# Kernel optimization log

Measured on AMD Instinct MI355X. Metric: run time of the kernel, lower is better.

## Reference

```python
import jax, jax.numpy as jnp
import numpy as np

D = 128      # state_dim
ED = 20      # edge_dim (RBF basis size)
R = 3        # num message/update rounds
G = 3        # gated equivariant blocks
CUT = 5.0    # cutoff
N = 10000    # nodes
E = 160000   # edges
B = 500      # molecules
HRO = 64     # readout hidden


def setup_inputs() -> dict:
    key = jax.random.key(0)
    ks = jax.random.split(key, 40)
    sc = 0.05

    def nrm(k, shape):
        return jax.random.normal(k, shape, dtype=jnp.float32) * sc

    inp = {
        "h": jax.random.normal(ks[0], (N, 5), dtype=jnp.float32),
        "pos": jax.random.normal(ks[1], (N, 3), dtype=jnp.float32),
        "edge_index": jax.random.randint(ks[2], (2, E), 0, N),
        "batch": jnp.sort(jax.random.randint(ks[3], (N,), 0, B)),
        # node embedding Linear(5, D)
        "emb_w": nrm(ks[4], (5, D)), "emb_b": nrm(ks[5], (D,)),
        # per-round message params (stacked over rounds)
        "msg_phi_w1": nrm(ks[6], (R, D, D)), "msg_phi_b1": nrm(ks[7], (R, D)),
        "msg_phi_w2": nrm(ks[8], (R, D, 3 * D)), "msg_phi_b2": nrm(ks[9], (R, 3 * D)),
        "msg_filt_w": nrm(ks[10], (R, ED, 3 * D)), "msg_filt_b": nrm(ks[11], (R, 3 * D)),
        # per-round update params
        "upd_U": nrm(ks[12], (R, D, D)), "upd_V": nrm(ks[13], (R, D, D)),
        "upd_w1": nrm(ks[14], (R, 2 * D, D)), "upd_b1": nrm(ks[15], (R, D)),
        "upd_w2": nrm(ks[16], (R, D, 3 * D)), "upd_b2": nrm(ks[17], (R, 3 * D)),
        # gated equivariant blocks
        "geb_wv1": nrm(ks[18], (G, D, D)), "geb_wv2": nrm(ks[19], (G, D, D)),
        "geb_w1": nrm(ks[20], (G, 2 * D, D)), "geb_b1": nrm(ks[21], (G, D)),
        "geb_w2": nrm(ks[22], (G, D, 2 * D)), "geb_b2": nrm(ks[23], (G, 2 * D)),
        # invariant readout MLP
        "ro_w1": nrm(ks[24], (D, HRO)), "ro_b1": nrm(ks[25], (HRO,)),
        "ro_w2": nrm(ks[26], (HRO, 1)), "ro_b2": nrm(ks[27], (1,)),
    }
    return inp


def _safe_norm(x, axis):
    return jnp.sqrt(jnp.sum(x * x, axis=axis) + 1e-8)


def reference(h, pos, edge_index, batch,
              emb_w, emb_b,
              msg_phi_w1, msg_phi_b1, msg_phi_w2, msg_phi_b2,
              msg_filt_w, msg_filt_b,
              upd_U, upd_V, upd_w1, upd_b1, upd_w2, upd_b2,
              geb_wv1, geb_wv2, geb_w1, geb_b1, geb_w2, geb_b2,
              ro_w1, ro_b1, ro_w2, ro_b2):
    n_nodes = h.shape[0]
    row, col = edge_index[0], edge_index[1]
    # edge vectors: r_ij = pos[col] - pos[row]
    r_ij = pos[col] - pos[row]                                   # [E,3]
    d = jnp.clip(jnp.linalg.norm(r_ij, axis=1, keepdims=True), 1e-6, None)  # [E,1]
    unit = r_ij / d                                              # [E,3]
    # sinc radial basis + cosine cutoff
    freqs = jnp.arange(1, ED + 1, dtype=h.dtype)
    rbf = jnp.sin(freqs * jnp.pi * d / CUT) / d                  # [E,ED]
    fcut = 0.5 * (jnp.cos(jnp.pi * d / CUT) + 1.0) * (d < CUT)   # [E,1]

    s = h @ emb_w + emb_b                                        # [N,D]
    v = jnp.zeros((n_nodes, D, 3), dtype=h.dtype)                # [N,D,3]

    for r in range(R):
        # --- PaiNNMessage ---
        phi = jax.nn.silu(s @ msg_phi_w1[r] + msg_phi_b1[r]) @ msg_phi_w2[r] + msg_phi_b2[r]  # [N,3D]
        filt = (rbf @ msg_filt_w[r] + msg_filt_b[r]) * fcut      # [E,3D]
        x = phi[col] * filt                                      # gather + modulate  [E,3D]
        xs, xvv, xvw = jnp.split(x, 3, axis=-1)                  # each [E,D]
        ds = jax.ops.segment_sum(xs, row, num_segments=n_nodes)  # [N,D]
        dv_e = xvv[:, :, None] * v[col] + xvw[:, :, None] * unit[:, None, :]  # [E,D,3]
        dv = jax.ops.segment_sum(dv_e, row, num_segments=n_nodes)             # [N,D,3]
        s = s + ds
        v = v + dv
        # --- PaiNNUpdate ---
        Uv = jnp.einsum('ndc,de->nec', v, upd_U[r])              # [N,D,3]
        Vv = jnp.einsum('ndc,de->nec', v, upd_V[r])              # [N,D,3]
        Vn = _safe_norm(Vv, axis=-1)                             # [N,D]
        a = jax.nn.silu(jnp.concatenate([s, Vn], axis=-1) @ upd_w1[r] + upd_b1[r]) @ upd_w2[r] + upd_b2[r]
        a_ss, a_sv, a_vv = jnp.split(a, 3, axis=-1)
        s = s + a_ss + a_sv * jnp.sum(Uv * Vv, axis=-1)
        v = v + a_vv[:, :, None] * Uv

    # --- GatedEquivariantBlocks ---
    for g in range(G):
        v1 = jnp.einsum('ndc,de->nec', v, geb_wv1[g])
        v2 = jnp.einsum('ndc,de->nec', v, geb_wv2[g])
        n2 = _safe_norm(v2, axis=-1)                             # [N,D]
        a = jax.nn.silu(jnp.concatenate([s, n2], axis=-1) @ geb_w1[g] + geb_b1[g]) @ geb_w2[g] + geb_b2[g]
        s_new, gate = jnp.split(a, 2, axis=-1)
        s = s_new
        v = gate[:, :, None] * v1

    # --- InvariantReadout + molwise scatter ---
    out = jax.nn.silu(s @ ro_w1 + ro_b1) @ ro_w2 + ro_b2         # [N,1]
    molwise = jax.ops.segment_sum(out, batch, num_segments=B)    # [B,1]
    return molwise.squeeze(-1)
```

## Files before the change

### kernel.cpp

```cpp
#include <hip/hip_runtime.h>

typedef __attribute__((ext_vector_type(4))) float f32x4;
typedef __attribute__((ext_vector_type(8))) short short8;

#define D 128
#define D3 384
#define SLD 256
#define EDIM 20
#define KPAD 32
#define NR 3
#define NG 3
#define CUTOFF 5.0f
#define NNODES 10000
#define NEDGES 160000
#define NMOL 500
#define HROH 64
#define PI_F 3.14159265358979323846f

#define FBIAS 1
#define FSILU 2
#define FBF16O 4

static __device__ __forceinline__ float silu_f(float x) {
    return x / (1.0f + expf(-x));
}

static __device__ __forceinline__ ushort f2bf(float x) {
    uint u = __float_as_uint(x);
    uint r = (u + 0x7fffu + ((u >> 16) & 1u)) >> 16;
    return (ushort)r;
}
static __device__ __forceinline__ float bf2f(ushort h) {
    return __uint_as_float((uint)h << 16);
}
static __device__ __forceinline__ uint pack2(float a, float b) {
    return (uint)f2bf(a) | ((uint)f2bf(b) << 16);
}

#define TLR 64
#define TLC 64
#define KC 32
#define APAD 40
#define BPAD 36
#define CPAD 68

struct WSrc { const float* p[12]; };
#define WTOT 880640

__global__ __launch_bounds__(256) void wprep_k(WSrc ws, ushort* __restrict__ dh,
                                               ushort* __restrict__ dl)
{
    const int srcK[12] = {128,128, 20,128,128,256,128,128,128,256,128,128};
    const int dstK[12] = {128,128, 32,128,128,256,128,128,128,256,128,128};
    const int Mm[12]   = {128,384,384,128,128,128,384,128,128,128,256, 64};
    const int nm[12]   = {  3,  3,  3,  3,  3,  3,  3,  3,  3,  3,  3,  1};
    int i = blockIdx.x * 256 + threadIdx.x;
    if (i >= WTOT) return;
    int off = 0, seg = -1, loc = 0;
    #pragma unroll
    for (int s = 0; s < 12; ++s) {
        int sz = nm[s] * Mm[s] * dstK[s];
        if (seg < 0 && i < off + sz) { seg = s; loc = i - off; }
        off += sz;
    }
    int K = dstK[seg], M = Mm[seg], sK = srcK[seg];
    int mat = loc / (M * K);
    int rem = loc - mat * M * K;
    int m = rem / K, k = rem - m * K;
    float v = (k < sK) ? ws.p[seg][(size_t)(mat * sK + k) * M + m] : 0.f;
    ushort h = f2bf(v);
    dh[i] = h;
    dl[i] = f2bf(v - bf2f(h));
}

#define SEG_PHI_W1  0
#define SEG_PHI_W2  49152
#define SEG_FILT_W  196608
#define SEG_UPD_U   233472
#define SEG_UPD_V   282624
#define SEG_UPD_W1  331776
#define SEG_UPD_W2  430080
#define SEG_GEB_WV1 577536
#define SEG_GEB_WV2 626688
#define SEG_GEB_W1  675840
#define SEG_GEB_W2  774144
#define SEG_RO_W1   872448

template <int K1, int M2, bool OUTBF>
__global__ __launch_bounds__(256) void mlp_k(
    const float* __restrict__ A, int lda,
    const ushort* __restrict__ W1h, const ushort* __restrict__ W1l,
    const float* __restrict__ b1,
    const ushort* __restrict__ W2h, const ushort* __restrict__ W2l,
    const float* __restrict__ b2,
    float* __restrict__ C, ushort* __restrict__ Cbf, int N)
{
    __shared__ char SMB[27648 + 17408];
    ushort* Ah  = (ushort*)SMB;
    ushort* Al  = Ah + 1280;
    ushort* B1h = Ah + 2560;
    ushort* B1l = B1h + 4608;
    ushort* Hh  = (ushort*)(SMB + 27648);
    ushort* Hl  = Hh + 4352;

    const int tid = threadIdx.x;
    const int n0 = blockIdx.x * 32;
    const int w = tid >> 6;
    const int rt = w & 1;
    const int ch = w >> 1;
    const int lane = tid & 63;
    const int fr = lane & 15;
    const int kg = lane >> 4;
    const int arow = tid & 31;
    const int akq = (tid >> 5) * 4;
    const bool aok = (n0 + arow) < N;
    const float* Ar = A + (size_t)(n0 + arow) * lda;
    const int bcol = tid & 127;
    const int bhalf = tid >> 7;

    f32x4 acc1[4];
    #pragma unroll
    for (int t = 0; t < 4; ++t) acc1[t] = (f32x4){0.f, 0.f, 0.f, 0.f};

    for (int k0 = 0; k0 < K1; k0 += KC) {
        {
            float4 v = aok ? *(const float4*)(Ar + k0 + akq)
                           : make_float4(0.f, 0.f, 0.f, 0.f);
            ushort h0 = f2bf(v.x), h1 = f2bf(v.y), h2 = f2bf(v.z), h3 = f2bf(v.w);
            ushort l0 = f2bf(v.x - bf2f(h0)), l1 = f2bf(v.y - bf2f(h1));
            ushort l2 = f2bf(v.z - bf2f(h2)), l3 = f2bf(v.w - bf2f(h3));
            uint2 ph, pl;
            ph.x = (uint)h0 | ((uint)h1 << 16); ph.y = (uint)h2 | ((uint)h3 << 16);
            pl.x = (uint)l0 | ((uint)l1 << 16); pl.y = (uint)l2 | ((uint)l3 << 16);
            *(uint2*)(Ah + arow * APAD + akq) = ph;
            *(uint2*)(Al + arow * APAD + akq) = pl;
        }
        {
            const ushort* sh = W1h + (size_t)bcol * K1 + k0 + bhalf * 16;
            const ushort* sl = W1l + (size_t)bcol * K1 + k0 + bhalf * 16;
            ushort* dh = B1h + bcol * BPAD + bhalf * 16;
            ushort* dl = B1l + bcol * BPAD + bhalf * 16;
            uint4 v0 = *(const uint4*)sh;
            uint4 v1 = *(const uint4*)(sh + 8);
            *(uint2*)dh       = make_uint2(v0.x, v0.y);
            *(uint2*)(dh + 4) = make_uint2(v0.z, v0.w);
            *(uint2*)(dh + 8) = make_uint2(v1.x, v1.y);
            *(uint2*)(dh + 12)= make_uint2(v1.z, v1.w);
            uint4 u0 = *(const uint4*)sl;
            uint4 u1 = *(const uint4*)(sl + 8);
            *(uint2*)dl       = make_uint2(u0.x, u0.y);
            *(uint2*)(dl + 4) = make_uint2(u0.z, u0.w);
            *(uint2*)(dl + 8) = make_uint2(u1.x, u1.y);
            *(uint2*)(dl + 12)= make_uint2(u1.z, u1.w);
        }
        __syncthreads();
        short8 ah = *(const short8*)(Ah + (rt * 16 + fr) * APAD + kg * 8);
        short8 al = *(const short8*)(Al + (rt * 16 + fr) * APAD + kg * 8);
        #pragma unroll
        for (int t = 0; t < 4; ++t) {
            const ushort* bp = B1h + (ch * 64 + t * 16 + fr) * BPAD + kg * 8;
            const ushort* bq = B1l + (ch * 64 + t * 16 + fr) * BPAD + kg * 8;
            short8 bh, bl;
            ((uint2*)&bh)[0] = *(const uint2*)bp;
            ((uint2*)&bh)[1] = *(const uint2*)(bp + 4);
            ((uint2*)&bl)[0] = *(const uint2*)bq;
            ((uint2*)&bl)[1] = *(const uint2*)(bq + 4);
            acc1[t] = __builtin_amdgcn_mfma_f32_16x16x32_bf16(ah, bh, acc1[t], 0, 0, 0);
            acc1[t] = __builtin_amdgcn_mfma_f32_16x16x32_bf16(al, bh, acc1[t], 0, 0, 0);
            acc1[t] = __builtin_amdgcn_mfma_f32_16x16x32_bf16(ah, bl, acc1[t], 0, 0, 0);
        }
        __syncthreads();
    }
    #pragma unroll
    for (int t = 0; t < 4; ++t) {
        int colm = ch * 64 + t * 16 + fr;
        float b = b1[colm];
        #pragma unroll
        for (int r = 0; r < 4; ++r) {
            int row = rt * 16 + kg * 4 + r;
            float hv = silu_f(acc1[t][r] + b);
            ushort hh = f2bf(hv);
            Hh[row * 136 + colm] = hh;
            Hl[row * 136 + colm] = f2bf(hv - bf2f(hh));
        }
    }
    __syncthreads();

    ushort* B2h = (ushort*)SMB;
    ushort* B2l = B2h + 4608;
    const int NG2 = M2 / 128;
    for (int g = 0; g < NG2; ++g) {
        f32x4 acc2[4];
        #pragma unroll
        for (int t = 0; t < 4; ++t) acc2[t] = (f32x4){0.f, 0.f, 0.f, 0.f};
        for (int k0 = 0; k0 < D; k0 += KC) {
            {
                const ushort* sh = W2h + (size_t)(g * 128 + bcol) * D + k0 + bhalf * 16;
                const ushort* sl = W2l + (size_t)(g * 128 + bcol) * D + k0 + bhalf * 16;
                ushort* dh = B2h + bcol * BPAD + bhalf * 16;
                ushort* dl = B2l + bcol * BPAD + bhalf * 16;
                uint4 v0 = *(const uint4*)sh;
                uint4 v1 = *(const uint4*)(sh + 8);
                *(uint2*)dh       = make_uint2(v0.x, v0.y);
                *(uint2*)(dh + 4) = make_uint2(v0.z, v0.w);
                *(uint2*)(dh + 8) = make_uint2(v1.x, v1.y);
                *(uint2*)(dh + 12)= make_uint2(v1.z, v1.w);
                uint4 u0 = *(const uint4*)sl;
                uint4 u1 = *(const uint4*)(sl + 8);
                *(uint2*)dl       = make_uint2(u0.x, u0.y);
                *(uint2*)(dl + 4) = make_uint2(u0.z, u0.w);
                *(uint2*)(dl + 8) = make_uint2(u1.x, u1.y);
                *(uint2*)(dl + 12)= make_uint2(u1.z, u1.w);
            }
            __syncthreads();
            short8 ah, al;
            {
                const ushort* hp = Hh + (rt * 16 + fr) * 136 + k0 + kg * 8;
                const ushort* hq = Hl + (rt * 16 + fr) * 136 + k0 + kg * 8;
                ((uint2*)&ah)[0] = *(const uint2*)hp;
                ((uint2*)&ah)[1] = *(const uint2*)(hp + 4);
                ((uint2*)&al)[0] = *(const uint2*)hq;
                ((uint2*)&al)[1] = *(const uint2*)(hq + 4);
            }
            #pragma unroll
            for (int t = 0; t < 4; ++t) {
                const ushort* bp = B2h + (ch * 64 + t * 16 + fr) * BPAD + kg * 8;
                const ushort* bq = B2l + (ch * 64 + t * 16 + fr) * BPAD + kg * 8;
                short8 bh, bl;
                ((uint2*)&bh)[0] = *(const uint2*)bp;
                ((uint2*)&bh)[1] = *(const uint2*)(bp + 4);
                ((uint2*)&bl)[0] = *(const uint2*)bq;
                ((uint2*)&bl)[1] = *(const uint2*)(bq + 4);
                acc2[t] = __builtin_amdgcn_mfma_f32_16x16x32_bf16(ah, bh, acc2[t], 0, 0, 0);
                acc2[t] = __builtin_amdgcn_mfma_f32_16x16x32_bf16(al, bh, acc2[t], 0, 0, 0);
                acc2[t] = __builtin_amdgcn_mfma_f32_16x16x32_bf16(ah, bl, acc2[t], 0, 0, 0);
            }
            __syncthreads();
        }
        if (OUTBF) {
            float* Cs = (float*)SMB;
            #pragma unroll
            for (int t = 0; t < 4; ++t) {
                int colm = ch * 64 + t * 16 + fr;
                float b = b2[g * 128 + colm];
                #pragma unroll
                for (int r = 0; r < 4; ++r) {
                    int row = rt * 16 + kg * 4 + r;
                    Cs[row * CPAD + colm] = acc2[t][r] + b;
                }
            }
            __syncthreads();
            #pragma unroll
            for (int it = 0; it < 2; ++it) {
                int chunk = it * 256 + tid;
                int row = chunk >> 4;
                int c8 = (chunk & 15) * 8;
                int n = n0 + row;
                if (n < N) {
                    const float* src = Cs + row * CPAD + c8;
                    uint4 pk;
                    pk.x = pack2(src[0], src[1]);
                    pk.y = pack2(src[2], src[3]);
                    pk.z = pack2(src[4], src[5]);
                    pk.w = pack2(src[6], src[7]);
                    *(uint4*)(Cbf + (size_t)n * M2 + g * 128 + c8) = pk;
                }
            }
            __syncthreads();
        } else {
            #pragma unroll
            for (int t = 0; t < 4; ++t) {
                int colm = ch * 64 + t * 16 + fr;
                float b = b2[g * 128 + colm];
                #pragma unroll
                for (int r = 0; r < 4; ++r) {
                    int n = n0 + rt * 16 + kg * 4 + r;
                    if (n < N)
                        C[(size_t)n * M2 + g * 128 + colm] = acc2[t][r] + b;
                }
            }
        }
    }
}

__global__ __launch_bounds__(256) void gemm_k(
    const float* __restrict__ A, int lda,
    const ushort* __restrict__ Wh, const ushort* __restrict__ Wl, int ldk,
    const float* __restrict__ bias,
    float* __restrict__ C, ushort* __restrict__ Cbf, int ldc,
    int N, int K, int flags)
{
    const int n0 = blockIdx.x * TLR;
    const int m0 = blockIdx.y * TLC;
    __shared__ ushort SM[9728];
    ushort* Ah = SM;
    ushort* Al = SM + 2560;
    ushort* Bh = SM + 5120;
    ushort* Bl = SM + 7424;
    const int tid = threadIdx.x;
    const int arow = tid & 63;
    const int akq = (tid >> 6) * 4;
    const bool aok = (n0 + arow) < N;
    const float* Ar = A + (size_t)(n0 + arow) * lda;
    const int sm = tid & 63;
    const int sq = tid >> 6;
    const ushort* Wph = Wh + (size_t)(m0 + sm) * ldk + sq * 8;
    const ushort* Wpl = Wl + (size_t)(m0 + sm) * ldk + sq * 8;
    const int lane = tid & 63;
    const int wrow = (tid >> 6) * 16;
    const int fr = lane & 15;
    const int kg = lane >> 4;

    f32x4 acc[4];
    #pragma unroll
    for (int t = 0; t < 4; ++t) acc[t] = (f32x4){0.f, 0.f, 0.f, 0.f};

    for (int k0 = 0; k0 < K; k0 += KC) {
        #pragma unroll
        for (int half = 0; half < 2; ++half) {
            int kk = akq + half * 16;
            float4 v = aok ? *(const float4*)(Ar + k0 + kk)
                           : make_float4(0.f, 0.f, 0.f, 0.f);
            ushort h0 = f2bf(v.x), h1 = f2bf(v.y), h2 = f2bf(v.z), h3 = f2bf(v.w);
            ushort l0 = f2bf(v.x - bf2f(h0)), l1 = f2bf(v.y - bf2f(h1));
            ushort l2 = f2bf(v.z - bf2f(h2)), l3 = f2bf(v.w - bf2f(h3));
            uint2 ph, pl;
            ph.x = (uint)h0 | ((uint)h1 << 16); ph.y = (uint)h2 | ((uint)h3 << 16);
            pl.x = (uint)l0 | ((uint)l1 << 16); pl.y = (uint)l2 | ((uint)l3 << 16);
            *(uint2*)(Ah + arow * APAD + kk) = ph;
            *(uint2*)(Al + arow * APAD + kk) = pl;
        }
        {
            uint4 vh = *(const uint4*)(Wph + k0);
            uint4 vl = *(const uint4*)(Wpl + k0);
            ushort* dh = Bh + sm * BPAD + sq * 8;
            ushort* dl = Bl + sm * BPAD + sq * 8;
            *(uint2*)dh       = make_uint2(vh.x, vh.y);
            *(uint2*)(dh + 4) = make_uint2(vh.z, vh.w);
            *(uint2*)dl       = make_uint2(vl.x, vl.y);
            *(uint2*)(dl + 4) = make_uint2(vl.z, vl.w);
        }
        __syncthreads();
        short8 ah = *(const short8*)(Ah + (wrow + fr) * APAD + kg * 8);
        short8 al = *(const short8*)(Al + (wrow + fr) * APAD + kg * 8);
        #pragma unroll
        for (int t = 0; t < 4; ++t) {
            const ushort* bp = Bh + (t * 16 + fr) * BPAD + kg * 8;
            const ushort* bq = Bl + (t * 16 + fr) * BPAD + kg * 8;
            short8 bh, bl;
            ((uint2*)&bh)[0] = *(const uint2*)bp;
            ((uint2*)&bh)[1] = *(const uint2*)(bp + 4);
            ((uint2*)&bl)[0] = *(const uint2*)bq;
            ((uint2*)&bl)[1] = *(const uint2*)(bq + 4);
            acc[t] = __builtin_amdgcn_mfma_f32_16x16x32_bf16(ah, bh, acc[t], 0, 0, 0);
            acc[t] = __builtin_amdgcn_mfma_f32_16x16x32_bf16(al, bh, acc[t], 0, 0, 0);
            acc[t] = __builtin_amdgcn_mfma_f32_16x16x32_bf16(ah, bl, acc[t], 0, 0, 0);
        }
        __syncthreads();
    }

    #pragma unroll
    for (int t = 0; t < 4; ++t) {
        #pragma unroll
        for (int r = 0; r < 4; ++r) {
            int n = n0 + wrow + kg * 4 + r;
            if (n < N) {
                int m = m0 + t * 16 + fr;
                float val = acc[t][r];
                if (flags & FBIAS) val += bias[m];
                if (flags & FSILU) val = silu_f(val);
                C[(size_t)n * ldc + m] = val;
            }
        }
    }
}

__global__ __launch_bounds__(256) void filt_k(
    const float* __restrict__ RBFp,
    const ushort* __restrict__ Wfh,
    const float* __restrict__ bias,
    const float* __restrict__ uf_s,
    const int* __restrict__ col_s,
    const ushort* __restrict__ Pbf,
    ushort* __restrict__ X, int E)
{
    __shared__ ushort Ah[64 * APAD];
    __shared__ ushort Bs[D3 * BPAD];
    __shared__ float  Cs[64 * CPAD];
    __shared__ int    ColS[64];
    const int tid = threadIdx.x;
    const int e0 = blockIdx.x * 64;
    #pragma unroll
    for (int it = 0; it < 2; ++it) {
        int chunk = it * 256 + tid;
        int row = chunk >> 3;
        int kq = (chunk & 7) * 4;
        int e = e0 + row;
        float4 v = (e < E) ? *(const float4*)(RBFp + (size_t)e * KPAD + kq)
                           : make_float4(0.f, 0.f, 0.f, 0.f);
        uint2 ph;
        ph.x = pack2(v.x, v.y);
        ph.y = pack2(v.z, v.w);
        *(uint2*)(Ah + row * APAD + kq) = ph;
    }
    for (int m = tid; m < D3; m += 256) {
        const ushort* s = Wfh + (size_t)m * KPAD;
        ushort* dst = Bs + m * BPAD;
        #pragma unroll
        for (int q = 0; q < 2; ++q) {
            uint4 v = *(const uint4*)(s + q * 16);
            *(uint2*)(dst + q * 16)      = make_uint2(v.x, v.y);
            *(uint2*)(dst + q * 16 + 4)  = make_uint2(v.z, v.w);
            uint4 v2 = *(const uint4*)(s + q * 16 + 8);
            *(uint2*)(dst + q * 16 + 8)  = make_uint2(v2.x, v2.y);
            *(uint2*)(dst + q * 16 + 12) = make_uint2(v2.z, v2.w);
        }
    }
    if (tid < 64) {
        int e = e0 + tid;
        ColS[tid] = (e < E) ? col_s[e] : 0;
    }
    __syncthreads();

    const int lane = tid & 63;
    const int wrow = (tid >> 6) * 16;
    const int fr = lane & 15;
    const int kg = lane >> 4;
    short8 ah = *(const short8*)(Ah + (wrow + fr) * APAD + kg * 8);
    f32x4 acc[24];
    #pragma unroll
    for (int t = 0; t < 24; ++t) {
        const ushort* bp = Bs + (t * 16 + fr) * BPAD + kg * 8;
        short8 bh;
        ((uint2*)&bh)[0] = *(const uint2*)bp;
        ((uint2*)&bh)[1] = *(const uint2*)(bp + 4);
        acc[t] = __builtin_amdgcn_mfma_f32_16x16x32_bf16(
            ah, bh, (f32x4){0.f, 0.f, 0.f, 0.f}, 0, 0, 0);
    }
    float fc[4];
    #pragma unroll
    for (int r = 0; r < 4; ++r) {
        int e = e0 + wrow + kg * 4 + r;
        fc[r] = (e < E) ? uf_s[(size_t)e * 4 + 3] : 0.f;
    }
    for (int ct = 0; ct < 6; ++ct) {
        __syncthreads();
        #pragma unroll
        for (int tt = 0; tt < 4; ++tt) {
            int t = ct * 4 + tt;
            int colm = t * 16 + fr;
            float b = bias[colm];
            #pragma unroll
            for (int r = 0; r < 4; ++r) {
                int row = wrow + kg * 4 + r;
                Cs[row * CPAD + tt * 16 + fr] = (acc[t][r] + b) * fc[r];
            }
        }
        __syncthreads();
        #pragma unroll
        for (int it = 0; it < 2; ++it) {
            int chunk = it * 256 + tid;
            int row = chunk >> 3;
            int c8 = (chunk & 7) * 8;
            int e = e0 + row;
            if (e < E) {
                int mbase = ct * 64 + c8;
                int col = ColS[row];
                uint4 pg = *(const uint4*)(Pbf + (size_t)col * D3 + mbase);
                const float* src = Cs + row * CPAD + c8;
                uint4 pk;
                pk.x = pack2(src[0] * bf2f((ushort)(pg.x & 0xffff)),
                             src[1] * bf2f((ushort)(pg.x >> 16)));
                pk.y = pack2(src[2] * bf2f((ushort)(pg.y & 0xffff)),
                             src[3] * bf2f((ushort)(pg.y >> 16)));
                pk.z = pack2(src[4] * bf2f((ushort)(pg.z & 0xffff)),
                             src[5] * bf2f((ushort)(pg.z >> 16)));
                pk.w = pack2(src[6] * bf2f((ushort)(pg.w & 0xffff)),
                             src[7] * bf2f((ushort)(pg.w >> 16)));
                *(uint4*)(X + (size_t)e * D3 + mbase) = pk;
            }
        }
    }
}

template <bool WITHDOT>
__global__ __launch_bounds__(256) void uvn_k(
    const float* __restrict__ A,
    const ushort* __restrict__ WUh, const ushort* __restrict__ WUl,
    const ushort* __restrict__ WVh, const ushort* __restrict__ WVl,
    float* __restrict__ Uv,
    float* __restrict__ DOT,
    float* __restrict__ SX, int N)
{
    const int n0 = blockIdx.x * 32;
    const int m0 = blockIdx.y * 64;
    __shared__ ushort Ah[3][32 * APAD], Al[3][32 * APAD];
    __shared__ ushort Bh[2][64 * BPAD], Bl[2][64 * BPAD];
    const int tid = threadIdx.x;
    const int arow = tid & 31;
    const int akq = (tid >> 5) * 4;
    const bool aok = (n0 + arow) < N;
    const float* Ar = A + (size_t)(n0 + arow) * D3;
    const int sm = tid & 63;
    const int sq = tid >> 6;
    const int w = tid >> 6;
    const int rt = w & 1;
    const int ch = w >> 1;
    const int lane = tid & 63;
    const int fr = lane & 15;
    const int kg = lane >> 4;

    f32x4 acc[3][2][2];
    #pragma unroll
    for (int c = 0; c < 3; ++c)
        #pragma unroll
        for (int s = 0; s < 2; ++s)
            #pragma unroll
            for (int t = 0; t < 2; ++t) acc[c][s][t] = (f32x4){0.f, 0.f, 0.f, 0.f};

    for (int k0 = 0; k0 < D; k0 += KC) {
        #pragma unroll
        for (int c = 0; c < 3; ++c) {
            float4 v = aok ? *(const float4*)(Ar + c * D + k0 + akq)
                           : make_float4(0.f, 0.f, 0.f, 0.f);
            ushort h0 = f2bf(v.x), h1 = f2bf(v.y), h2 = f2bf(v.z), h3 = f2bf(v.w);
            ushort l0 = f2bf(v.x - bf2f(h0)), l1 = f2bf(v.y - bf2f(h1));
            ushort l2 = f2bf(v.z - bf2f(h2)), l3 = f2bf(v.w - bf2f(h3));
            uint2 ph, pl;
            ph.x = (uint)h0 | ((uint)h1 << 16); ph.y = (uint)h2 | ((uint)h3 << 16);
            pl.x = (uint)l0 | ((uint)l1 << 16); pl.y = (uint)l2 | ((uint)l3 << 16);
            *(uint2*)(&Ah[c][arow * APAD + akq]) = ph;
            *(uint2*)(&Al[c][arow * APAD + akq]) = pl;
        }
        #pragma unroll
        for (int s = 0; s < 2; ++s) {
            const ushort* sh = (s ? WVh : WUh) + (size_t)(m0 + sm) * D + k0 + sq * 8;
            const ushort* sl = (s ? WVl : WUl) + (size_t)(m0 + sm) * D + k0 + sq * 8;
            uint4 vh = *(const uint4*)sh;
            uint4 vl = *(const uint4*)sl;
            ushort* dh = &Bh[s][sm * BPAD + sq * 8];
            ushort* dl = &Bl[s][sm * BPAD + sq * 8];
            *(uint2*)dh       = make_uint2(vh.x, vh.y);
            *(uint2*)(dh + 4) = make_uint2(vh.z, vh.w);
            *(uint2*)dl       = make_uint2(vl.x, vl.y);
            *(uint2*)(dl + 4) = make_uint2(vl.z, vl.w);
        }
        __syncthreads();
        short8 ah[3], al[3];
        #pragma unroll
        for (int c = 0; c < 3; ++c) {
            ah[c] = *(const short8*)(&Ah[c][(rt * 16 + fr) * APAD + kg * 8]);
            al[c] = *(const short8*)(&Al[c][(rt * 16 + fr) * APAD + kg * 8]);
        }
        #pragma unroll
        for (int t = 0; t < 2; ++t) {
            #pragma unroll
            for (int s = 0; s < 2; ++s) {
                const ushort* bp = &Bh[s][(ch * 32 + t * 16 + fr) * BPAD + kg * 8];
                const ushort* bq = &Bl[s][(ch * 32 + t * 16 + fr) * BPAD + kg * 8];
                short8 bh, bl;
                ((uint2*)&bh)[0] = *(const uint2*)bp;
                ((uint2*)&bh)[1] = *(const uint2*)(bp + 4);
                ((uint2*)&bl)[0] = *(const uint2*)bq;
                ((uint2*)&bl)[1] = *(const uint2*)(bq + 4);
                #pragma unroll
                for (int c = 0; c < 3; ++c) {
                    acc[c][s][t] = __builtin_amdgcn_mfma_f32_16x16x32_bf16(ah[c], bh, acc[c][s][t], 0, 0, 0);
                    acc[c][s][t] = __builtin_amdgcn_mfma_f32_16x16x32_bf16(al[c], bh, acc[c][s][t], 0, 0, 0);
                    acc[c][s][t] = __builtin_amdgcn_mfma_f32_16x16x32_bf16(ah[c], bl, acc[c][s][t], 0, 0, 0);
                }
            }
        }
        __syncthreads();
    }
    #pragma unroll
    for (int t = 0; t < 2; ++t) {
        #pragma unroll
        for (int r = 0; r < 4; ++r) {
            int n = n0 + rt * 16 + kg * 4 + r;
            if (n < N) {
                int m = m0 + ch * 32 + t * 16 + fr;
                float ux = acc[0][0][t][r], uy = acc[1][0][t][r], uz = acc[2][0][t][r];
                float vx = acc[0][1][t][r], vy = acc[1][1][t][r], vz = acc[2][1][t][r];
                float* up = Uv + (size_t)n * D3 + m;
                up[0]     = ux;
                up[D]     = uy;
                up[2 * D] = uz;
                SX[(size_t)n * SLD + D + m] =
                    sqrtf(fmaf(vx, vx, fmaf(vy, vy, fmaf(vz, vz, 1e-8f))));
                if (WITHDOT)
                    DOT[(size_t)n * D + m] = fmaf(ux, vx, fmaf(uy, vy, uz * vz));
            }
        }
    }
}

__global__ __launch_bounds__(256) void emb_k(
    const float* __restrict__ h, const float* __restrict__ w,
    const float* __restrict__ b, float* __restrict__ s, int total)
{
    int i = blockIdx.x * 256 + threadIdx.x;
    if (i >= total) return;
    int n = i >> 7, d = i & 127;
    float acc = b[d];
    #pragma unroll
    for (int k = 0; k < 5; ++k) acc = fmaf(h[n * 5 + k], w[k * D + d], acc);
    s[(size_t)n * SLD + d] = acc;
}

__global__ __launch_bounds__(256) void hist_k(const int* __restrict__ ei,
                                              int* __restrict__ cnt, int E)
{
    int e = blockIdx.x * 256 + threadIdx.x;
    if (e < E) atomicAdd(&cnt[ei[e]], 1);
}

__global__ __launch_bounds__(256) void scan_k(const int* __restrict__ cnt,
                                              int* __restrict__ offs, int n)
{
    __shared__ int tmp[256];
    __shared__ int carry;
    if (threadIdx.x == 0) carry = 0;
    __syncthreads();
    for (int base = 0; base < n; base += 256) {
        int i = base + threadIdx.x;
        int v = (i < n) ? cnt[i] : 0;
        tmp[threadIdx.x] = v;
        __syncthreads();
        for (int off = 1; off < 256; off <<= 1) {
            int add = (threadIdx.x >= off) ? tmp[threadIdx.x - off] : 0;
            __syncthreads();
            tmp[threadIdx.x] += add;
            __syncthreads();
        }
        if (i < n) offs[i + 1] = carry + tmp[threadIdx.x];
        __syncthreads();
        if (threadIdx.x == 255) carry += tmp[255];
        __syncthreads();
    }
    if (threadIdx.x == 0) offs[0] = 0;
}

__global__ __launch_bounds__(256) void initnext_k(const int* __restrict__ offs,
                                                  int* __restrict__ next, int n)
{
    int i = blockIdx.x * 256 + threadIdx.x;
    if (i < n) next[i] = offs[i];
}

__global__ __launch_bounds__(256) void edge_pre_k(
    const int* __restrict__ ei, const float* __restrict__ pos,
    int* __restrict__ next, float* __restrict__ rbf_s,
    float* __restrict__ uf_s, int* __restrict__ col_s, int E)
{
    int e = blockIdx.x * 256 + threadIdx.x;
    if (e >= E) return;
    int r = ei[e], c = ei[E + e];
    float dx = pos[c * 3 + 0] - pos[r * 3 + 0];
    float dy = pos[c * 3 + 1] - pos[r * 3 + 1];
    float dz = pos[c * 3 + 2] - pos[r * 3 + 2];
    float dist = sqrtf(dx * dx + dy * dy + dz * dz);
    float d = fmaxf(dist, 1e-6f);
    float inv = 1.0f / d;
    int p = atomicAdd(&next[r], 1);
    col_s[p] = c;
    uf_s[p * 4 + 0] = dx * inv;
    uf_s[p * 4 + 1] = dy * inv;
    uf_s[p * 4 + 2] = dz * inv;
    uf_s[p * 4 + 3] = (d < CUTOFF) ? 0.5f * (cosf(PI_F * d / CUTOFF) + 1.0f) : 0.0f;
    float w = PI_F * d / CUTOFF;
    float* rb = rbf_s + (size_t)p * KPAD;
    #pragma unroll
    for (int k = 1; k <= EDIM; ++k)
        rb[k - 1] = sinf((float)k * w) * inv;
    #pragma unroll
    for (int k = EDIM; k < KPAD; ++k) rb[k] = 0.f;
}

#define MSG_NPB 2
__global__ __launch_bounds__(256) void message_csr_k(
    const int* __restrict__ offs, const int* __restrict__ col_s,
    const ushort* __restrict__ X, const float* __restrict__ uf_s,
    const float* __restrict__ Vold, const ushort* __restrict__ VbfOld,
    float* __restrict__ S, float* __restrict__ Vnew,
    ushort* __restrict__ VbfNew, int N)
{
    const int sub = threadIdx.x >> 7;
    const int d = threadIdx.x & 127;

    auto edge = [&](int j, float& ds, float& dvx, float& dvy, float& dvz) {
        const ushort* xp = X + (size_t)j * D3;
        float xs  = bf2f(xp[d]);
        float xvv = bf2f(xp[D + d]);
        float xvw = bf2f(xp[2 * D + d]);
        int col = col_s[j];
        float4 u4 = *(const float4*)(uf_s + (size_t)j * 4);
        const ushort* vc = VbfOld + (size_t)col * D3;
        ds += xs;
        dvx = fmaf(xvv, bf2f(vc[d]),         fmaf(xvw, u4.x, dvx));
        dvy = fmaf(xvv, bf2f(vc[D + d]),     fmaf(xvw, u4.y, dvy));
        dvz = fmaf(xvv, bf2f(vc[2 * D + d]), fmaf(xvw, u4.z, dvz));
    };

    int n = blockIdx.x * MSG_NPB + sub;
    if (n >= N) return;
    float ds0 = 0.f, dx0 = 0.f, dy0 = 0.f, dz0 = 0.f;
    float ds1 = 0.f, dx1 = 0.f, dy1 = 0.f, dz1 = 0.f;
    const int j0 = offs[n], j1 = offs[n + 1];
    int j = j0;
    for (; j + 2 <= j1; j += 2) {
        edge(j, ds0, dx0, dy0, dz0);
        edge(j + 1, ds1, dx1, dy1, dz1);
    }
    if (j < j1) edge(j, ds0, dx0, dy0, dz0);
    S[(size_t)n * SLD + d] += ds0 + ds1;
    const float* vo = Vold + (size_t)n * D3;
    float* vn = Vnew + (size_t)n * D3;
    ushort* vb = VbfNew + (size_t)n * D3;
    float nx = vo[d] + dx0 + dx1;
    float ny = vo[D + d] + dy0 + dy1;
    float nz = vo[2 * D + d] + dz0 + dz1;
    vn[d] = nx;         vb[d] = f2bf(nx);
    vn[D + d] = ny;     vb[D + d] = f2bf(ny);
    vn[2 * D + d] = nz; vb[2 * D + d] = f2bf(nz);
}

__global__ __launch_bounds__(256) void upd_apply_k(
    const float* __restrict__ U3, const float* __restrict__ DOT,
    const float* __restrict__ P, float* __restrict__ s,
    float* __restrict__ v, ushort* __restrict__ vbf, int total)
{
    int i = blockIdx.x * 256 + threadIdx.x;
    if (i >= total) return;
    int n = i >> 7, d = i & 127;
    const float* u = U3 + (size_t)n * D3;
    float ux = u[d], uy = u[D + d], uz = u[2 * D + d];
    const float* a = P + (size_t)n * D3;
    s[(size_t)n * SLD + d] += a[d] + a[D + d] * DOT[i];
    float avv = a[2 * D + d];
    float* vv = v + (size_t)n * D3;
    ushort* vb = vbf + (size_t)n * D3;
    float nx = fmaf(avv, ux, vv[d]);
    float ny = fmaf(avv, uy, vv[D + d]);
    float nz = fmaf(avv, uz, vv[2 * D + d]);
    vv[d] = nx;         vb[d] = f2bf(nx);
    vv[D + d] = ny;     vb[D + d] = f2bf(ny);
    vv[2 * D + d] = nz; vb[2 * D + d] = f2bf(nz);
}

__global__ __launch_bounds__(256) void geb_apply_k(
    const float* __restrict__ P, const float* __restrict__ U3,
    float* __restrict__ s, float* __restrict__ v, int total)
{
    int i = blockIdx.x * 256 + threadIdx.x;
    if (i >= total) return;
    int n = i >> 7, d = i & 127;
    const float* a = P + (size_t)n * 2 * D;
    s[(size_t)n * SLD + d] = a[d];
    float g = a[D + d];
    const float* u = U3 + (size_t)n * D3;
    float* vv = v + (size_t)n * D3;
    vv[d]         = g * u[d];
    vv[D + d]     = g * u[D + d];
    vv[2 * D + d] = g * u[2 * D + d];
}

__global__ __launch_bounds__(256) void readout_k(
    const float* __restrict__ H2, const float* __restrict__ w2,
    const float* __restrict__ b2, const int* __restrict__ batch,
    float* __restrict__ out, int N)
{
    int n = blockIdx.x * 256 + threadIdx.x;
    if (n >= N) return;
    float acc = b2[0];
    const float* hrow = H2 + (size_t)n * HROH;
    #pragma unroll
    for (int k = 0; k < HROH; ++k) acc = fmaf(hrow[k], w2[k], acc);
    atomicAdd(out + batch[n], acc);
}


extern "C" void kernel_launch(void* const* d_in, const int* in_sizes, int n_in,
                              void* d_out, int out_size, void* d_ws, size_t ws_size,
                              hipStream_t stream)
{
    const float* h          = (const float*)d_in[0];
    const float* pos        = (const float*)d_in[1];
    const int*   ei         = (const int*)d_in[2];
    const int*   batch      = (const int*)d_in[3];
    const float* emb_w      = (const float*)d_in[4];
    const float* emb_b      = (const float*)d_in[5];
    const float* msg_phi_w1 = (const float*)d_in[6];
    const float* msg_phi_b1 = (const float*)d_in[7];
    const float* msg_phi_w2 = (const float*)d_in[8];
    const float* msg_phi_b2 = (const float*)d_in[9];
    const float* msg_filt_w = (const float*)d_in[10];
    const float* msg_filt_b = (const float*)d_in[11];
    const float* upd_U      = (const float*)d_in[12];
    const float* upd_V      = (const float*)d_in[13];
    const float* upd_w1     = (const float*)d_in[14];
    const float* upd_b1     = (const float*)d_in[15];
    const float* upd_w2     = (const float*)d_in[16];
    const float* upd_b2     = (const float*)d_in[17];
    const float* geb_wv1    = (const float*)d_in[18];
    const float* geb_wv2    = (const float*)d_in[19];
    const float* geb_w1     = (const float*)d_in[20];
    const float* geb_b1     = (const float*)d_in[21];
    const float* geb_w2     = (const float*)d_in[22];
    const float* geb_b2     = (const float*)d_in[23];
    const float* ro_w1      = (const float*)d_in[24];
    const float* ro_b1      = (const float*)d_in[25];
    const float* ro_w2      = (const float*)d_in[26];
    const float* ro_b2      = (const float*)d_in[27];
    float* out = (float*)d_out;

    const int N = NNODES, E = NEDGES;

    char* p = (char*)d_ws;
    auto carve = [&](size_t bytes) {
        char* r = p;
        p += (bytes + 255) & ~(size_t)255;
        return r;
    };
    float*  SX   = (float*)carve((size_t)N * SLD * 4);
    float*  VA   = (float*)carve((size_t)N * D3 * 4);
    float*  VB   = (float*)carve((size_t)N * D3 * 4);
    float*  P_   = (float*)carve((size_t)N * D3 * 4);
    ushort* Pbf  = (ushort*)P_;
    ushort* VBFa = (ushort*)carve((size_t)N * D3 * 2);
    ushort* VBFb = (ushort*)carve((size_t)N * D3 * 2);
    float*  H    = (float*)carve((size_t)N * D * 4);
    float*  H2   = (float*)carve((size_t)N * D * 4);
    float*  RBFp = (float*)carve((size_t)E * KPAD * 4);
    float*  UFs  = (float*)carve((size_t)E * 4 * 4);
    int*    COLs = (int*)carve((size_t)E * 4);
    int*    offs = (int*)carve((size_t)(N + 1) * 4);
    int*    nxt  = (int*)carve((size_t)N * 4);
    ushort* WTH  = (ushort*)carve((size_t)WTOT * 2);
    ushort* WTL  = (ushort*)carve((size_t)WTOT * 2);
    ushort* X    = (ushort*)carve((size_t)E * D3 * 2);

    WSrc wsrc;
    wsrc.p[0] = msg_phi_w1; wsrc.p[1] = msg_phi_w2; wsrc.p[2] = msg_filt_w;
    wsrc.p[3] = upd_U;      wsrc.p[4] = upd_V;      wsrc.p[5] = upd_w1;
    wsrc.p[6] = upd_w2;     wsrc.p[7] = geb_wv1;    wsrc.p[8] = geb_wv2;
    wsrc.p[9] = geb_w1;     wsrc.p[10] = geb_w2;    wsrc.p[11] = ro_w1;
    hipLaunchKernelGGL(wprep_k, dim3((WTOT + 255) / 256), dim3(256), 0, stream,
                       wsrc, WTH, WTL);

    hipMemsetAsync(VA, 0, (size_t)N * D3 * 4, stream);
    hipMemsetAsync(VBFa, 0, (size_t)N * D3 * 2, stream);
    hipLaunchKernelGGL(emb_k, dim3((N * D + 255) / 256), dim3(256), 0, stream,
                       h, emb_w, emb_b, SX, N * D);
    hipMemsetAsync(nxt, 0, (size_t)N * 4, stream);
    hipLaunchKernelGGL(hist_k, dim3((E + 255) / 256), dim3(256), 0, stream, ei, nxt, E);
    hipLaunchKernelGGL(scan_k, dim3(1), dim3(256), 0, stream, nxt, offs, N);
    hipLaunchKernelGGL(initnext_k, dim3((N + 255) / 256), dim3(256), 0, stream,
                       offs, nxt, N);
    hipLaunchKernelGGL(edge_pre_k, dim3((E + 255) / 256), dim3(256), 0, stream,
                       ei, pos, nxt, RBFp, UFs, COLs, E);

    float*  Vc = VA;   ushort* VbfC = VBFa;
    float*  Vs = VB;   ushort* VbfS = VBFb;
    const int MB = (N + 31) / 32;

    for (int r = 0; r < NR; ++r) {
        hipLaunchKernelGGL(HIP_KERNEL_NAME(mlp_k<128, 384, true>),
                           dim3(MB), dim3(256), 0, stream,
                           SX, SLD,
                           WTH + SEG_PHI_W1 + (size_t)r * D * D,
                           WTL + SEG_PHI_W1 + (size_t)r * D * D,
                           msg_phi_b1 + (size_t)r * D,
                           WTH + SEG_PHI_W2 + (size_t)r * D * D3,
                           WTL + SEG_PHI_W2 + (size_t)r * D * D3,
                           msg_phi_b2 + (size_t)r * D3,
                           nullptr, Pbf, N);
        hipLaunchKernelGGL(filt_k, dim3((E + 63) / 64), dim3(256), 0, stream,
                           RBFp, WTH + SEG_FILT_W + (size_t)r * KPAD * D3,
                           msg_filt_b + (size_t)r * D3, UFs, COLs, Pbf, X, E);
        hipLaunchKernelGGL(message_csr_k, dim3((N + MSG_NPB - 1) / MSG_NPB),
                           dim3(256), 0, stream,
                           offs, COLs, X, UFs, Vc, VbfC, SX, Vs, VbfS, N);
        { float* t = Vc; Vc = Vs; Vs = t; }
        { ushort* t = VbfC; VbfC = VbfS; VbfS = t; }
        float* Uv = Vs;
        hipLaunchKernelGGL(HIP_KERNEL_NAME(uvn_k<true>),
                           dim3(MB, 2), dim3(256), 0, stream,
                           Vc, WTH + SEG_UPD_U + (size_t)r * D * D,
                           WTL + SEG_UPD_U + (size_t)r * D * D,
                           WTH + SEG_UPD_V + (size_t)r * D * D,
                           WTL + SEG_UPD_V + (size_t)r * D * D,
                           Uv, H, SX, N);
        hipLaunchKernelGGL(HIP_KERNEL_NAME(mlp_k<256, 384, false>),
                           dim3(MB), dim3(256), 0, stream,
                           SX, SLD,
                           WTH + SEG_UPD_W1 + (size_t)r * 2 * D * D,
                           WTL + SEG_UPD_W1 + (size_t)r * 2 * D * D,
                           upd_b1 + (size_t)r * D,
                           WTH + SEG_UPD_W2 + (size_t)r * D * D3,
                           WTL + SEG_UPD_W2 + (size_t)r * D * D3,
                           upd_b2 + (size_t)r * D3,
                           P_, nullptr, N);
        hipLaunchKernelGGL(upd_apply_k, dim3((N * D + 255) / 256), dim3(256), 0,
                           stream, Uv, H, P_, SX, Vc, VbfC, N * D);
    }

    for (int g = 0; g < NG; ++g) {
        float* Uv = Vs;
        hipLaunchKernelGGL(HIP_KERNEL_NAME(uvn_k<false>),
                           dim3(MB, 2), dim3(256), 0, stream,
                           Vc, WTH + SEG_GEB_WV1 + (size_t)g * D * D,
                           WTL + SEG_GEB_WV1 + (size_t)g * D * D,
                           WTH + SEG_GEB_WV2 + (size_t)g * D * D,
                           WTL + SEG_GEB_WV2 + (size_t)g * D * D,
                           Uv, nullptr, SX, N);
        hipLaunchKernelGGL(HIP_KERNEL_NAME(mlp_k<256, 256, false>),
                           dim3(MB), dim3(256), 0, stream,
                           SX, SLD,
                           WTH + SEG_GEB_W1 + (size_t)g * 2 * D * D,
                           WTL + SEG_GEB_W1 + (size_t)g * 2 * D * D,
                           geb_b1 + (size_t)g * D,
                           WTH + SEG_GEB_W2 + (size_t)g * D * 2 * D,
                           WTL + SEG_GEB_W2 + (size_t)g * D * 2 * D,
                           geb_b2 + (size_t)g * 2 * D,
                           P_, nullptr, N);
        hipLaunchKernelGGL(geb_apply_k, dim3((N * D + 255) / 256), dim3(256), 0,
                           stream, P_, Uv, SX, Vc, N * D);
    }

    {
        dim3 grd((N + TLR - 1) / TLR, HROH / TLC > 0 ? HROH / TLC : 1, 1);
        hipLaunchKernelGGL(gemm_k, grd, dim3(256), 0, stream,
                           SX, SLD, WTH + SEG_RO_W1, WTL + SEG_RO_W1, D,
                           ro_b1, H2, nullptr, HROH, N, D, FBIAS | FSILU);
    }
    hipMemsetAsync(out, 0, (size_t)NMOL * 4, stream);
    hipLaunchKernelGGL(readout_k, dim3((N + 255) / 256), dim3(256), 0, stream,
                       H2, ro_w2, ro_b2, batch, out, N);
}
```

Baseline: 849.2 us.

## Fuse update/gate apply into MLP epilogue and use bf16 vectors in uvn

Removes the separate upd_apply and geb_apply elementwise kernels by applying the scalar and vector updates directly in the second-GEMM epilogue of mlp_k, avoiding the intermediate P buffer round trip and extra launches. uvn_k now reads the precomputed bf16 copy of v instead of splitting fp32 into hi/lo parts, dropping one MFMA pass and halving A loads. This reduces accuracy of the U/V projections to single-bf16 input precision, and the fused epilogue uses uncoalesced strided stores.

```diff
diff --git a/kernel.cpp b/kernel.cpp
--- a/kernel.cpp
+++ b/kernel.cpp
@@ -19,7 +19,6 @@
 
 #define FBIAS 1
 #define FSILU 2
-#define FBF16O 4
 
 static __device__ __forceinline__ float silu_f(float x) {
     return x / (1.0f + expf(-x));
@@ -86,14 +85,17 @@
 #define SEG_GEB_W2  774144
 #define SEG_RO_W1   872448
 
-template <int K1, int M2, bool OUTBF>
+template <int K1, int M2, int MODE>
 __global__ __launch_bounds__(256) void mlp_k(
     const float* __restrict__ A, int lda,
     const ushort* __restrict__ W1h, const ushort* __restrict__ W1l,
     const float* __restrict__ b1,
     const ushort* __restrict__ W2h, const ushort* __restrict__ W2l,
     const float* __restrict__ b2,
-    float* __restrict__ C, ushort* __restrict__ Cbf, int N)
+    ushort* __restrict__ Cbf,
+    float* __restrict__ SXp, const float* __restrict__ Uv,
+    const float* __restrict__ DOT,
+    float* __restrict__ V, ushort* __restrict__ Vbf, int N)
 {
     __shared__ char SMB[27648 + 17408];
     ushort* Ah  = (ushort*)SMB;
@@ -237,7 +239,7 @@
             }
             __syncthreads();
         }
-        if (OUTBF) {
+        if (MODE == 1) {
             float* Cs = (float*)SMB;
             #pragma unroll
             for (int t = 0; t < 4; ++t) {
@@ -267,6 +269,34 @@
                 }
             }
             __syncthreads();
+        } else if (MODE == 2) {
+            #pragma unroll
+            for (int t = 0; t < 4; ++t) {
+                int colm = ch * 64 + t * 16 + fr;
+                float b = b2[g * 128 + colm];
+                #pragma unroll
+                for (int r = 0; r < 4; ++r) {
+                    int n = n0 + rt * 16 + kg * 4 + r;
+                    if (n >= N) continue;
+                    float val = acc2[t][r] + b;
+                    if (g == 0) {
+                        SXp[(size_t)n * SLD + colm] += val;
+                    } else if (g == 1) {
+                        SXp[(size_t)n * SLD + colm] +=
+                            val * DOT[(size_t)n * D + colm];
+                    } else {
+                        const float* u = Uv + (size_t)n * D3 + colm;
+                        float* vv = V + (size_t)n * D3 + colm;
+                        ushort* vb = Vbf + (size_t)n * D3 + colm;
+                        float nx = fmaf(val, u[0],     vv[0]);
+                        float ny = fmaf(val, u[D],     vv[D]);
+                        float nz = fmaf(val, u[2 * D], vv[2 * D]);
+                        vv[0] = nx;     vb[0] = f2bf(nx);
+                        vv[D] = ny;     vb[D] = f2bf(ny);
+                        vv[2 * D] = nz; vb[2 * D] = f2bf(nz);
+                    }
+                }
+            }
         } else {
             #pragma unroll
             for (int t = 0; t < 4; ++t) {
@@ -275,8 +305,21 @@
                 #pragma unroll
                 for (int r = 0; r < 4; ++r) {
                     int n = n0 + rt * 16 + kg * 4 + r;
-                    if (n < N)
-                        C[(size_t)n * M2 + g * 128 + colm] = acc2[t][r] + b;
+                    if (n >= N) continue;
+                    float val = acc2[t][r] + b;
+                    if (g == 0) {
+                        SXp[(size_t)n * SLD + colm] = val;
+                    } else {
+                        const float* u = Uv + (size_t)n * D3 + colm;
+                        float* vv = V + (size_t)n * D3 + colm;
+                        ushort* vb = Vbf + (size_t)n * D3 + colm;
+                        float nx = val * u[0];
+                        float ny = val * u[D];
+                        float nz = val * u[2 * D];
+                        vv[0] = nx;     vb[0] = f2bf(nx);
+                        vv[D] = ny;     vb[D] = f2bf(ny);
+                        vv[2 * D] = nz; vb[2 * D] = f2bf(nz);
+                    }
                 }
             }
         }
@@ -287,8 +330,7 @@
     const float* __restrict__ A, int lda,
     const ushort* __restrict__ Wh, const ushort* __restrict__ Wl, int ldk,
     const float* __restrict__ bias,
-    float* __restrict__ C, ushort* __restrict__ Cbf, int ldc,
-    int N, int K, int flags)
+    float* __restrict__ C, int ldc, int N, int K, int flags)
 {
     const int n0 = blockIdx.x * TLR;
     const int m0 = blockIdx.y * TLC;
@@ -485,7 +527,7 @@
 
 template <bool WITHDOT>
 __global__ __launch_bounds__(256) void uvn_k(
-    const float* __restrict__ A,
+    const ushort* __restrict__ Abf,
     const ushort* __restrict__ WUh, const ushort* __restrict__ WUl,
     const ushort* __restrict__ WVh, const ushort* __restrict__ WVl,
     float* __restrict__ Uv,
@@ -494,13 +536,13 @@
 {
     const int n0 = blockIdx.x * 32;
     const int m0 = blockIdx.y * 64;
-    __shared__ ushort Ah[3][32 * APAD], Al[3][32 * APAD];
+    __shared__ ushort Ah[3][32 * APAD];
     __shared__ ushort Bh[2][64 * BPAD], Bl[2][64 * BPAD];
     const int tid = threadIdx.x;
     const int arow = tid & 31;
     const int akq = (tid >> 5) * 4;
     const bool aok = (n0 + arow) < N;
-    const float* Ar = A + (size_t)(n0 + arow) * D3;
+    const ushort* Ar = Abf + (size_t)(n0 + arow) * D3;
     const int sm = tid & 63;
     const int sq = tid >> 6;
     const int w = tid >> 6;
@@ -521,16 +563,9 @@
     for (int k0 = 0; k0 < D; k0 += KC) {
         #pragma unroll
         for (int c = 0; c < 3; ++c) {
-            float4 v = aok ? *(const float4*)(Ar + c * D + k0 + akq)
-                           : make_float4(0.f, 0.f, 0.f, 0.f);
-            ushort h0 = f2bf(v.x), h1 = f2bf(v.y), h2 = f2bf(v.z), h3 = f2bf(v.w);
-            ushort l0 = f2bf(v.x - bf2f(h0)), l1 = f2bf(v.y - bf2f(h1));
-            ushort l2 = f2bf(v.z - bf2f(h2)), l3 = f2bf(v.w - bf2f(h3));
-            uint2 ph, pl;
-            ph.x = (uint)h0 | ((uint)h1 << 16); ph.y = (uint)h2 | ((uint)h3 << 16);
-            pl.x = (uint)l0 | ((uint)l1 << 16); pl.y = (uint)l2 | ((uint)l3 << 16);
-            *(uint2*)(&Ah[c][arow * APAD + akq]) = ph;
-            *(uint2*)(&Al[c][arow * APAD + akq]) = pl;
+            uint2 v = aok ? *(const uint2*)(Ar + c * D + k0 + akq)
+                          : make_uint2(0, 0);
+            *(uint2*)(&Ah[c][arow * APAD + akq]) = v;
         }
         #pragma unroll
         for (int s = 0; s < 2; ++s) {
@@ -546,12 +581,10 @@
             *(uint2*)(dl + 4) = make_uint2(vl.z, vl.w);
         }
         __syncthreads();
-        short8 ah[3], al[3];
-        #pragma unroll
-        for (int c = 0; c < 3; ++c) {
+        short8 ah[3];
+        #pragma unroll
+        for (int c = 0; c < 3; ++c)
             ah[c] = *(const short8*)(&Ah[c][(rt * 16 + fr) * APAD + kg * 8]);
-            al[c] = *(const short8*)(&Al[c][(rt * 16 + fr) * APAD + kg * 8]);
-        }
         #pragma unroll
         for (int t = 0; t < 2; ++t) {
             #pragma unroll
@@ -566,7 +599,6 @@
                 #pragma unroll
                 for (int c = 0; c < 3; ++c) {
                     acc[c][s][t] = __builtin_amdgcn_mfma_f32_16x16x32_bf16(ah[c], bh, acc[c][s][t], 0, 0, 0);
-                    acc[c][s][t] = __builtin_amdgcn_mfma_f32_16x16x32_bf16(al[c], bh, acc[c][s][t], 0, 0, 0);
                     acc[c][s][t] = __builtin_amdgcn_mfma_f32_16x16x32_bf16(ah[c], bl, acc[c][s][t], 0, 0, 0);
                 }
             }
@@ -723,46 +755,6 @@
     vn[d] = nx;         vb[d] = f2bf(nx);
     vn[D + d] = ny;     vb[D + d] = f2bf(ny);
     vn[2 * D + d] = nz; vb[2 * D + d] = f2bf(nz);
-}
-
-__global__ __launch_bounds__(256) void upd_apply_k(
-    const float* __restrict__ U3, const float* __restrict__ DOT,
-    const float* __restrict__ P, float* __restrict__ s,
-    float* __restrict__ v, ushort* __restrict__ vbf, int total)
-{
-    int i = blockIdx.x * 256 + threadIdx.x;
-    if (i >= total) return;
-    int n = i >> 7, d = i & 127;
-    const float* u = U3 + (size_t)n * D3;
-    float ux = u[d], uy = u[D + d], uz = u[2 * D + d];
-    const float* a = P + (size_t)n * D3;
-    s[(size_t)n * SLD + d] += a[d] + a[D + d] * DOT[i];
-    float avv = a[2 * D + d];
-    float* vv = v + (size_t)n * D3;
-    ushort* vb = vbf + (size_t)n * D3;
-    float nx = fmaf(avv, ux, vv[d]);
-    float ny = fmaf(avv, uy, vv[D + d]);
-    float nz = fmaf(avv, uz, vv[2 * D + d]);
-    vv[d] = nx;         vb[d] = f2bf(nx);
-    vv[D + d] = ny;     vb[D + d] = f2bf(ny);
-    vv[2 * D + d] = nz; vb[2 * D + d] = f2bf(nz);
-}
-
-__global__ __launch_bounds__(256) void geb_apply_k(
-    const float* __restrict__ P, const float* __restrict__ U3,
-    float* __restrict__ s, float* __restrict__ v, int total)
-{
-    int i = blockIdx.x * 256 + threadIdx.x;
-    if (i >= total) return;
-    int n = i >> 7, d = i & 127;
-    const float* a = P + (size_t)n * 2 * D;
-    s[(size_t)n * SLD + d] = a[d];
-    float g = a[D + d];
-    const float* u = U3 + (size_t)n * D3;
-    float* vv = v + (size_t)n * D3;
-    vv[d]         = g * u[d];
-    vv[D + d]     = g * u[D + d];
-    vv[2 * D + d] = g * u[2 * D + d];
 }
 
 __global__ __launch_bounds__(256) void readout_k(
@@ -865,7 +857,7 @@
     const int MB = (N + 31) / 32;
 
     for (int r = 0; r < NR; ++r) {
-        hipLaunchKernelGGL(HIP_KERNEL_NAME(mlp_k<128, 384, true>),
+        hipLaunchKernelGGL(HIP_KERNEL_NAME(mlp_k<128, 384, 1>),
                            dim3(MB), dim3(256), 0, stream,
                            SX, SLD,
                            WTH + SEG_PHI_W1 + (size_t)r * D * D,
@@ -874,7 +866,7 @@
                            WTH + SEG_PHI_W2 + (size_t)r * D * D3,
                            WTL + SEG_PHI_W2 + (size_t)r * D * D3,
                            msg_phi_b2 + (size_t)r * D3,
-                           nullptr, Pbf, N);
+                           Pbf, nullptr, nullptr, nullptr, nullptr, nullptr, N);
         hipLaunchKernelGGL(filt_k, dim3((E + 63) / 64), dim3(256), 0, stream,
                            RBFp, WTH + SEG_FILT_W + (size_t)r * KPAD * D3,
                            msg_filt_b + (size_t)r * D3, UFs, COLs, Pbf, X, E);
@@ -886,12 +878,12 @@
         float* Uv = Vs;
         hipLaunchKernelGGL(HIP_KERNEL_NAME(uvn_k<true>),
                            dim3(MB, 2), dim3(256), 0, stream,
-                           Vc, WTH + SEG_UPD_U + (size_t)r * D * D,
+                           VbfC, WTH + SEG_UPD_U + (size_t)r * D * D,
                            WTL + SEG_UPD_U + (size_t)r * D * D,
                            WTH + SEG_UPD_V + (size_t)r * D * D,
                            WTL + SEG_UPD_V + (size_t)r * D * D,
                            Uv, H, SX, N);
-        hipLaunchKernelGGL(HIP_KERNEL_NAME(mlp_k<256, 384, false>),
+        hipLaunchKernelGGL(HIP_KERNEL_NAME(mlp_k<256, 384, 2>),
                            dim3(MB), dim3(256), 0, stream,
                            SX, SLD,
                            WTH + SEG_UPD_W1 + (size_t)r * 2 * D * D,
@@ -900,21 +892,19 @@
                            WTH + SEG_UPD_W2 + (size_t)r * D * D3,
                            WTL + SEG_UPD_W2 + (size_t)r * D * D3,
                            upd_b2 + (size_t)r * D3,
-                           P_, nullptr, N);
-        hipLaunchKernelGGL(upd_apply_k, dim3((N * D + 255) / 256), dim3(256), 0,
-                           stream, Uv, H, P_, SX, Vc, VbfC, N * D);
+                           nullptr, SX, Uv, H, Vc, VbfC, N);
     }
 
     for (int g = 0; g < NG; ++g) {
         float* Uv = Vs;
         hipLaunchKernelGGL(HIP_KERNEL_NAME(uvn_k<false>),
                            dim3(MB, 2), dim3(256), 0, stream,
-                           Vc, WTH + SEG_GEB_WV1 + (size_t)g * D * D,
+                           VbfC, WTH + SEG_GEB_WV1 + (size_t)g * D * D,
                            WTL + SEG_GEB_WV1 + (size_t)g * D * D,
                            WTH + SEG_GEB_WV2 + (size_t)g * D * D,
                            WTL + SEG_GEB_WV2 + (size_t)g * D * D,
                            Uv, nullptr, SX, N);
-        hipLaunchKernelGGL(HIP_KERNEL_NAME(mlp_k<256, 256, false>),
+        hipLaunchKernelGGL(HIP_KERNEL_NAME(mlp_k<256, 256, 3>),
                            dim3(MB), dim3(256), 0, stream,
                            SX, SLD,
                            WTH + SEG_GEB_W1 + (size_t)g * 2 * D * D,
@@ -923,16 +913,14 @@
                            WTH + SEG_GEB_W2 + (size_t)g * D * 2 * D,
                            WTL + SEG_GEB_W2 + (size_t)g * D * 2 * D,
                            geb_b2 + (size_t)g * 2 * D,
-                           P_, nullptr, N);
-        hipLaunchKernelGGL(geb_apply_k, dim3((N * D + 255) / 256), dim3(256), 0,
-                           stream, P_, Uv, SX, Vc, N * D);
+                           nullptr, SX, Uv, nullptr, Vc, VbfC, N);
     }
 
     {
-        dim3 grd((N + TLR - 1) / TLR, HROH / TLC > 0 ? HROH / TLC : 1, 1);
+        dim3 grd((N + TLR - 1) / TLR, 1, 1);
         hipLaunchKernelGGL(gemm_k, grd, dim3(256), 0, stream,
                            SX, SLD, WTH + SEG_RO_W1, WTL + SEG_RO_W1, D,
-                           ro_b1, H2, nullptr, HROH, N, D, FBIAS | FSILU);
+                           ro_b1, H2, HROH, N, D, FBIAS | FSILU);
     }
     hipMemsetAsync(out, 0, (size_t)NMOL * 4, stream);
     hipLaunchKernelGGL(readout_k, dim3((N + 255) / 256), dim3(256), 0, stream,
```

New measurement: 836.9 us. No clear change (-1.4%).
